# Optimization experiments

Hardware: AMD Instinct MI355X
Metric: run time of the kernel (lower is better)

Reference implementation:

```python
import jax, jax.numpy as jnp
import numpy as np

N_USER, N_PC, N_URL = 200000, 50000, 100000
E_USES, E_VISITS = 1000000, 1000000
H = 64
NUM_LAYERS = 2


def setup_inputs() -> dict:
    key = jax.random.key(0)
    ks = jax.random.split(key, 32)
    ki = iter(ks)

    def nrm(shape, scale=0.1):
        return jax.random.normal(next(ki), shape, dtype=jnp.float32) * scale

    inp = {
        "x_user": jax.random.normal(next(ki), (N_USER, 6), dtype=jnp.float32),
        "x_pc": jax.random.normal(next(ki), (N_PC, 4), dtype=jnp.float32),
        "x_url": jax.random.normal(next(ki), (N_URL, 3), dtype=jnp.float32),
        # edge_uses: row0 = user src ids, row1 = pc dst ids
        "edge_uses": jnp.stack([
            jax.random.randint(next(ki), (E_USES,), 0, N_USER),
            jax.random.randint(next(ki), (E_USES,), 0, N_PC),
        ]).astype(jnp.int32),
        # edge_visits: row0 = user src ids, row1 = url dst ids
        "edge_visits": jnp.stack([
            jax.random.randint(next(ki), (E_VISITS,), 0, N_USER),
            jax.random.randint(next(ki), (E_VISITS,), 0, N_URL),
        ]).astype(jnp.int32),
        # input projections (PyG Linear: y = x @ W + b)
        "Wu": nrm((6, H)), "bu": nrm((H,)),
        "Wp": nrm((4, H)), "bp": nrm((H,)),
        "Wl": nrm((3, H)), "bl": nrm((H,)),
        # per layer, per relation SAGEConv params; relation order:
        # 0: user-uses->pc, 1: pc-used_by->user, 2: user-visits->url, 3: url-visited_by->user
        "sage_l_W": nrm((NUM_LAYERS, 4, H, H)),
        "sage_l_b": nrm((NUM_LAYERS, 4, H)),
        "sage_r_W": nrm((NUM_LAYERS, 4, H, H)),
        # classifier (dropout is identity at eval)
        "cW1": nrm((H, H // 2)), "cb1": nrm((H // 2,)),
        "cW2": nrm((H // 2, 2)), "cb2": nrm((2,)),
    }
    return inp


def _sage(x_src, x_dst, src_idx, dst_idx, W_l, b_l, W_r, n_dst):
    # SAGEConv: lin_l(mean_{neighbors} x_src) + lin_r(x_dst)
    msg = x_src[src_idx]                                   # [E, H] gather
    s = jax.ops.segment_sum(msg, dst_idx, num_segments=n_dst)
    cnt = jax.ops.segment_sum(jnp.ones((src_idx.shape[0],), jnp.float32),
                              dst_idx, num_segments=n_dst)[:, None]
    mean = jnp.where(cnt > 0, s / jnp.maximum(cnt, 1.0), 0.0)
    return mean @ W_l + b_l + x_dst @ W_r


def reference(x_user, x_pc, x_url, edge_uses, edge_visits,
              Wu, bu, Wp, bp, Wl, bl,
              sage_l_W, sage_l_b, sage_r_W,
              cW1, cb1, cW2, cb2):
    hu = x_user @ Wu + bu
    hp = x_pc @ Wp + bp
    hl = x_url @ Wl + bl

    u2p_s, u2p_d = edge_uses[0], edge_uses[1]
    u2l_s, u2l_d = edge_visits[0], edge_visits[1]

    for layer in range(NUM_LAYERS):
        WL, BL, WR = sage_l_W[layer], sage_l_b[layer], sage_r_W[layer]
        new_pc = _sage(hu, hp, u2p_s, u2p_d, WL[0], BL[0], WR[0], N_PC)
        new_user = (_sage(hp, hu, u2p_d, u2p_s, WL[1], BL[1], WR[1], N_USER)
                    + _sage(hl, hu, u2l_d, u2l_s, WL[3], BL[3], WR[3], N_USER))
        new_url = _sage(hu, hl, u2l_s, u2l_d, WL[2], BL[2], WR[2], N_URL)
        hu, hp, hl = jax.nn.relu(new_user), jax.nn.relu(new_pc), jax.nn.relu(new_url)

    h = jax.nn.relu(hu @ cW1 + cb1)
    return h @ cW2 + cb2
```

## Files before the change

kernel.cpp:

```cpp
#include <hip/hip_runtime.h>

typedef __attribute__((ext_vector_type(8))) short bf16x8;
typedef __attribute__((ext_vector_type(4))) float f32x4;
typedef __attribute__((ext_vector_type(4))) int i32x4;
typedef unsigned short u16;

constexpr int NUSER = 200000;
constexpr int NPC   = 50000;
constexpr int NURL  = 100000;
constexpr int EUSES = 1000000;
constexpr int EVIS  = 1000000;
constexpr int HD    = 64;
constexpr int ETOT2 = 2 * (EUSES + EVIS);

constexpr int SB_P  = 0;
constexpr int SB_U1 = NPC;
constexpr int SB_L  = NPC + NUSER;
constexpr int SB_U2 = NPC + NUSER + NURL;
constexpr int NTOT  = NPC + NUSER + NURL + NUSER;

constexpr int CAP_P = 56;
constexpr int CAP_U = 28;
constexpr int CAP_L = 36;

constexpr int NBIN  = 128;
constexpr int NBINS = 512;
constexpr int NSCB  = 256;
constexpr int NSCAN = NBINS * NSCB;

__device__ __forceinline__ int binOfP(int k) { return (k * NBIN) / NPC; }
__device__ __forceinline__ int binOfU(int k) { return (k * NBIN) / NUSER; }
__device__ __forceinline__ int binOfL(int k) { return (k * NBIN) / NURL; }

__device__ __forceinline__ u16 f2bf(float f) {
    union { float f; unsigned u; } v; v.f = f;
    unsigned r = v.u + 0x7fff + ((v.u >> 16) & 1);
    return (u16)(r >> 16);
}
__device__ __forceinline__ float bf2f(u16 b) {
    union { unsigned u; float f; } v; v.u = ((unsigned)b) << 16; return v.f;
}
__device__ __forceinline__ void acc8(float* a, uint4 v) {
    unsigned w0 = v.x, w1 = v.y, w2 = v.z, w3 = v.w;
    a[0] += bf2f((u16)(w0 & 0xffff)); a[1] += bf2f((u16)(w0 >> 16));
    a[2] += bf2f((u16)(w1 & 0xffff)); a[3] += bf2f((u16)(w1 >> 16));
    a[4] += bf2f((u16)(w2 & 0xffff)); a[5] += bf2f((u16)(w2 >> 16));
    a[6] += bf2f((u16)(w3 & 0xffff)); a[7] += bf2f((u16)(w3 >> 16));
}


__global__ __launch_bounds__(256) void proj_k(
    const float* __restrict__ x, const float* __restrict__ W,
    const float* __restrict__ b, u16* __restrict__ h,
    int n, int din)
{
    int id = blockIdx.x * 256 + threadIdx.x;
    int node = id >> 6, c = id & 63;
    if (node >= n) return;
    float acc = b[c];
    for (int k = 0; k < din; ++k)
        acc += x[node * din + k] * W[k * 64 + c];
    h[id] = f2bf(acc);
}

__global__ __launch_bounds__(256) void bin_count_k(
    const int* __restrict__ eu, const int* __restrict__ ev,
    int* __restrict__ blockCnt)
{
    __shared__ int hist[NBINS];
    int tid = threadIdx.x;
    for (int i = tid; i < NBINS; i += 256) hist[i] = 0;
    __syncthreads();
    int stride = gridDim.x * 256;
    for (int e = blockIdx.x * 256 + tid; e < EUSES; e += stride) {
        int s = __builtin_nontemporal_load(eu + e);
        int d = __builtin_nontemporal_load(eu + EUSES + e);
        atomicAdd(&hist[binOfP(d)], 1);
        atomicAdd(&hist[NBIN + binOfU(s)], 1);
    }
    for (int e = blockIdx.x * 256 + tid; e < EVIS; e += stride) {
        int s = __builtin_nontemporal_load(ev + e);
        int d = __builtin_nontemporal_load(ev + EVIS + e);
        atomicAdd(&hist[2 * NBIN + binOfL(d)], 1);
        atomicAdd(&hist[3 * NBIN + binOfU(s)], 1);
    }
    __syncthreads();
    for (int i = tid; i < NBINS; i += 256)
        blockCnt[i * NSCB + blockIdx.x] = hist[i];
}

__global__ __launch_bounds__(256) void scanA_k(
    const int* __restrict__ in, int* __restrict__ out,
    int* __restrict__ bsum, int n)
{
    __shared__ int lds[256];
    int b = blockIdx.x, t = threadIdx.x;
    int base = b * 1024 + t * 4;
    int v[4]; int s = 0;
    #pragma unroll
    for (int i = 0; i < 4; ++i) { v[i] = (base + i < n) ? in[base + i] : 0; s += v[i]; }
    int x = s;
    lds[t] = x; __syncthreads();
    for (int off = 1; off < 256; off <<= 1) {
        int y = (t >= off) ? lds[t - off] : 0;
        __syncthreads();
        x += y; lds[t] = x;
        __syncthreads();
    }
    int excl = x - s;
    #pragma unroll
    for (int i = 0; i < 4; ++i) { if (base + i < n) out[base + i] = excl; excl += v[i]; }
    if (t == 255) bsum[b] = x;
}

__global__ __launch_bounds__(256) void scanB_k(int* __restrict__ bsum, int nb)
{
    __shared__ int lds[256];
    int t = threadIdx.x;
    int carry = 0;
    for (int base = 0; base < nb; base += 256) {
        int i = base + t;
        int s = (i < nb) ? bsum[i] : 0;
        int x = s;
        lds[t] = x; __syncthreads();
        for (int off = 1; off < 256; off <<= 1) {
            int y = (t >= off) ? lds[t - off] : 0;
            __syncthreads();
            x += y; lds[t] = x;
            __syncthreads();
        }
        if (i < nb) bsum[i] = carry + x - s;
        int tot = lds[255];
        __syncthreads();
        carry += tot;
    }
}

__global__ __launch_bounds__(256) void scanC_k(
    int* __restrict__ out, const int* __restrict__ bsum, int n)
{
    int i = blockIdx.x * 256 + threadIdx.x;
    if (i >= n) return;
    out[i] += bsum[i >> 10];
}

__global__ __launch_bounds__(256) void bin_scatter_k(
    const int* __restrict__ eu, const int* __restrict__ ev,
    const int* __restrict__ blockScan, int2* __restrict__ binned)
{
    __shared__ int base[NBINS];
    __shared__ int cur[NBINS];
    int tid = threadIdx.x;
    for (int i = tid; i < NBINS; i += 256) {
        base[i] = blockScan[i * NSCB + blockIdx.x];
        cur[i] = 0;
    }
    __syncthreads();
    int stride = gridDim.x * 256;
    for (int e = blockIdx.x * 256 + tid; e < EUSES; e += stride) {
        int s = __builtin_nontemporal_load(eu + e);
        int d = __builtin_nontemporal_load(eu + EUSES + e);
        int b0 = binOfP(d);
        int r0 = atomicAdd(&cur[b0], 1);
        binned[(size_t)base[b0] + r0] = make_int2(d, s);
        int b1 = NBIN + binOfU(s);
        int r1 = atomicAdd(&cur[b1], 1);
        binned[(size_t)base[b1] + r1] = make_int2(s, d);
    }
    for (int e = blockIdx.x * 256 + tid; e < EVIS; e += stride) {
        int s = __builtin_nontemporal_load(ev + e);
        int d = __builtin_nontemporal_load(ev + EVIS + e);
        int b2 = 2 * NBIN + binOfL(d);
        int r2 = atomicAdd(&cur[b2], 1);
        binned[(size_t)base[b2] + r2] = make_int2(d, s);
        int b3 = 3 * NBIN + binOfU(s);
        int r3 = atomicAdd(&cur[b3], 1);
        binned[(size_t)base[b3] + r3] = make_int2(s, d);
    }
}

__global__ __launch_bounds__(256) void bucket_build_k(
    const int2* __restrict__ binned, const int* __restrict__ blockScan,
    int* __restrict__ deg,
    int* __restrict__ colP, int* __restrict__ colU1,
    int* __restrict__ colL, int* __restrict__ colU2)
{
    __shared__ int ldsDeg[1568];
    int bin = blockIdx.x;
    int rel = bin >> 7, sub = bin & (NBIN - 1);
    int tid = threadIdx.x;
    int range, slot0, cap;
    int* col;
    if (rel == 0)      { range = NPC;   slot0 = SB_P;  col = colP;  cap = CAP_P; }
    else if (rel == 1) { range = NUSER; slot0 = SB_U1; col = colU1; cap = CAP_U; }
    else if (rel == 2) { range = NURL;  slot0 = SB_L;  col = colL;  cap = CAP_L; }
    else               { range = NUSER; slot0 = SB_U2; col = colU2; cap = CAP_U; }
    int lo = (sub * range + NBIN - 1) / NBIN;
    int hi = ((sub + 1) * range + NBIN - 1) / NBIN;
    int nk = hi - lo;
    for (int i = tid; i < nk; i += 256) ldsDeg[i] = 0;
    __syncthreads();
    int b0 = blockScan[bin * NSCB];
    int bend = (bin == NBINS - 1) ? ETOT2 : blockScan[(bin + 1) * NSCB];
    int cnt = bend - b0;
    for (int i = tid; i < cnt; i += 256) {
        int2 kp = binned[(size_t)b0 + i];
        int r = atomicAdd(&ldsDeg[kp.x - lo], 1);
        if (r < cap) col[(size_t)kp.x * cap + r] = kp.y;
    }
    __syncthreads();
    for (int i = tid; i < nk; i += 256) deg[slot0 + lo + i] = ldsDeg[i];
}

__global__ __launch_bounds__(256) void gather_all_k(
    const u16* __restrict__ hu, const u16* __restrict__ hp,
    const u16* __restrict__ hl,
    const int* __restrict__ colP, const int* __restrict__ colU1,
    const int* __restrict__ colL, const int* __restrict__ colU2,
    const int* __restrict__ deg, u16* __restrict__ meanAll)
{
    int t = blockIdx.x * 256 + threadIdx.x;
    int slot = t >> 3;
    if (slot >= NTOT) return;
    int lane8 = (t & 7) << 3;
    const u16* hsrc;
    const int* col;
    int cap;
    if (slot < SB_U1)      { hsrc = hu; col = colP  + (size_t)(slot)         * CAP_P; cap = CAP_P; }
    else if (slot < SB_L)  { hsrc = hp; col = colU1 + (size_t)(slot - SB_U1) * CAP_U; cap = CAP_U; }
    else if (slot < SB_U2) { hsrc = hu; col = colL  + (size_t)(slot - SB_L)  * CAP_L; cap = CAP_L; }
    else                   { hsrc = hl; col = colU2 + (size_t)(slot - SB_U2) * CAP_U; cap = CAP_U; }
    int dg = deg[slot];
    int m_n = dg < cap ? dg : cap;
    float a[8] = {0.f,0.f,0.f,0.f,0.f,0.f,0.f,0.f};
    const i32x4* colv = (const i32x4*)col;
    int nb = m_n >> 2, rem = m_n & 3;
    if (m_n > 0) {
        i32x4 c = __builtin_nontemporal_load(colv);
        for (int b = 0; b < nb; ++b) {
            i32x4 cn = __builtin_nontemporal_load(colv + b + 1);
            uint4 v0 = *(const uint4*)(hsrc + (size_t)c[0] * 64 + lane8);
            uint4 v1 = *(const uint4*)(hsrc + (size_t)c[1] * 64 + lane8);
            uint4 v2 = *(const uint4*)(hsrc + (size_t)c[2] * 64 + lane8);
            uint4 v3 = *(const uint4*)(hsrc + (size_t)c[3] * 64 + lane8);
            acc8(a, v0); acc8(a, v1); acc8(a, v2); acc8(a, v3);
            c = cn;
        }
        if (rem > 0) { uint4 v = *(const uint4*)(hsrc + (size_t)c[0] * 64 + lane8); acc8(a, v); }
        if (rem > 1) { uint4 v = *(const uint4*)(hsrc + (size_t)c[1] * 64 + lane8); acc8(a, v); }
        if (rem > 2) { uint4 v = *(const uint4*)(hsrc + (size_t)c[2] * 64 + lane8); acc8(a, v); }
    }
    float inv = dg > 0 ? 1.f / (float)dg : 0.f;
    uint4 m;
    m.x = (unsigned)f2bf(a[0] * inv) | ((unsigned)f2bf(a[1] * inv) << 16);
    m.y = (unsigned)f2bf(a[2] * inv) | ((unsigned)f2bf(a[3] * inv) << 16);
    m.z = (unsigned)f2bf(a[4] * inv) | ((unsigned)f2bf(a[5] * inv) << 16);
    m.w = (unsigned)f2bf(a[6] * inv) | ((unsigned)f2bf(a[7] * inv) << 16);
    *(uint4*)(meanAll + (size_t)slot * 64 + lane8) = m;
}

__global__ __launch_bounds__(256) void btprep_k(
    const float* __restrict__ lW, const float* __restrict__ lB,
    const float* __restrict__ rW,
    u16* __restrict__ bt, float* __restrict__ bias)
{
    int idx = blockIdx.x * 256 + threadIdx.x;
    if (idx < 57344) {
        int layer = idx / 28672, rem = idx % 28672;
        size_t wb = (size_t)layer * 4 * 4096;
        int n, k, K; float val; u16* out;
        if (rem < 8192) {
            K = 128; n = rem >> 7; k = rem & 127;
            val = k < 64 ? lW[wb + 0 * 4096 + k * 64 + n]
                         : rW[wb + 0 * 4096 + (k - 64) * 64 + n];
            out = bt + (size_t)layer * 28672;
        } else if (rem < 16384) {
            int e = rem - 8192; K = 128; n = e >> 7; k = e & 127;
            val = k < 64 ? lW[wb + 2 * 4096 + k * 64 + n]
                         : rW[wb + 2 * 4096 + (k - 64) * 64 + n];
            out = bt + (size_t)layer * 28672 + 8192;
        } else {
            int e = rem - 16384; K = 192; n = e / 192; k = e % 192;
            if (k < 64)       val = lW[wb + 1 * 4096 + k * 64 + n];
            else if (k < 128) val = lW[wb + 3 * 4096 + (k - 64) * 64 + n];
            else              val = rW[wb + 1 * 4096 + (k - 128) * 64 + n]
                                  + rW[wb + 3 * 4096 + (k - 128) * 64 + n];
            out = bt + (size_t)layer * 28672 + 16384;
        }
        int byte = n * (2 * K) + 2 * k;
        byte ^= ((n & 7) << 4);
        out[byte >> 1] = f2bf(val);
    } else if (idx < 57728) {
        int i2 = idx - 57344;
        int layer = i2 / 192, r = i2 % 192, which = r / 64, c = r % 64;
        size_t bb = (size_t)layer * 4 * 64;
        float v;
        if (which == 0)      v = lB[bb + 0 * 64 + c];
        else if (which == 1) v = lB[bb + 2 * 64 + c];
        else                 v = lB[bb + 1 * 64 + c] + lB[bb + 3 * 64 + c];
        bias[(layer * 3 + which) * 64 + c] = v;
    }
}

template<int STEPS>
__global__ __launch_bounds__(256) void sage_mfma_k(
    const u16* __restrict__ src0, const u16* __restrict__ src1,
    const u16* __restrict__ src2, u16* __restrict__ hout,
    const u16* __restrict__ Bt, const float* __restrict__ bias, int n)
{
    constexpr int K = STEPS * 32;
    __shared__ u16 sB[64 * K];
    int tid = threadIdx.x;
    for (int i = tid; i < 64 * K / 8; i += 256)
        ((uint4*)sB)[i] = ((const uint4*)Bt)[i];
    __syncthreads();

    int lane = tid & 63, wave = tid >> 6;
    int row0 = blockIdx.x * 64 + wave * 16;
    int arow = row0 + (lane & 15);
    int kq = (lane >> 4) * 8;
    bool rowok = arow < n;

    const u16* srcs[3] = {src0, src1, src2};
    f32x4 acc0 = {0.f,0.f,0.f,0.f}, acc1 = acc0, acc2 = acc0, acc3 = acc0;
    f32x4* acc[4] = {&acc0, &acc1, &acc2, &acc3};

    #pragma unroll
    for (int s = 0; s < STEPS; ++s) {
        const u16* sp = srcs[s >> 1];
        int klocal = (s & 1) * 32 + kq;
        bf16x8 afrag = {0,0,0,0,0,0,0,0};
        if (rowok) afrag = *(const bf16x8*)(sp + (size_t)arow * 64 + klocal);
        int kk = s * 32 + kq;
        #pragma unroll
        for (int t = 0; t < 4; ++t) {
            int colc = t * 16 + (lane & 15);
            int byte = colc * (2 * K) + kk * 2;
            byte ^= ((colc & 7) << 4);
            bf16x8 bfrag = *(const bf16x8*)((const char*)sB + byte);
            *acc[t] = __builtin_amdgcn_mfma_f32_16x16x32_bf16(afrag, bfrag, *acc[t], 0, 0, 0);
        }
    }

    #pragma unroll
    for (int t = 0; t < 4; ++t) {
        int colc = t * 16 + (lane & 15);
        float bs = bias[colc];
        #pragma unroll
        for (int r = 0; r < 4; ++r) {
            int row = row0 + (lane >> 4) * 4 + r;
            if (row < n)
                hout[(size_t)row * 64 + colc] = f2bf(fmaxf((*acc[t])[r] + bs, 0.f));
        }
    }
}

__global__ __launch_bounds__(256) void classifier_k(
    const u16* __restrict__ hu,
    const float* __restrict__ cW1, const float* __restrict__ cb1,
    const float* __restrict__ cW2, const float* __restrict__ cb2,
    float* __restrict__ out, int n)
{
    __shared__ float sW1[64 * 32];
    __shared__ float sX[32][65];
    __shared__ float sHid[32][33];
    __shared__ float sW2[64];
    __shared__ float sb1[32];
    __shared__ float sb2[2];
    int tid = threadIdx.x;
    for (int i = tid; i < 2048; i += 256) sW1[i] = cW1[i];
    if (tid < 64) sW2[tid] = cW2[tid];
    if (tid < 32) sb1[tid] = cb1[tid];
    if (tid < 2)  sb2[tid] = cb2[tid];
    int row0 = blockIdx.x * 32;
    {
        int r = tid >> 3, k8 = (tid & 7) * 8;
        int gr = row0 + r;
        if (gr < n) {
            uint4 v = *(const uint4*)(hu + (size_t)gr * 64 + k8);
            unsigned w[4] = {v.x, v.y, v.z, v.w};
            #pragma unroll
            for (int j = 0; j < 4; ++j) {
                sX[r][k8 + 2 * j]     = bf2f((u16)(w[j] & 0xffff));
                sX[r][k8 + 2 * j + 1] = bf2f((u16)(w[j] >> 16));
            }
        } else {
            #pragma unroll
            for (int j = 0; j < 8; ++j) sX[r][k8 + j] = 0.f;
        }
    }
    __syncthreads();
    int c  = tid & 31;
    int rb = tid >> 5;
    for (int r = rb; r < 32; r += 8) {
        float acc = sb1[c];
        #pragma unroll
        for (int k = 0; k < 64; ++k) acc += sX[r][k] * sW1[k * 32 + c];
        sHid[r][c] = fmaxf(acc, 0.f);
    }
    __syncthreads();
    if (tid < 64) {
        int r = tid >> 1, j = tid & 1;
        int gr = row0 + r;
        if (gr < n) {
            float acc = sb2[j];
            #pragma unroll
            for (int k = 0; k < 32; ++k) acc += sHid[r][k] * sW2[k * 2 + j];
            out[gr * 2 + j] = acc;
        }
    }
}

extern "C" void kernel_launch(void* const* d_in, const int* in_sizes, int n_in,
                              void* d_out, int out_size, void* d_ws, size_t ws_size,
                              hipStream_t stream)
{
    const float* x_user = (const float*)d_in[0];
    const float* x_pc   = (const float*)d_in[1];
    const float* x_url  = (const float*)d_in[2];
    const int*   e_uses = (const int*)d_in[3];
    const int*   e_vis  = (const int*)d_in[4];
    const float* Wu = (const float*)d_in[5];
    const float* bu = (const float*)d_in[6];
    const float* Wp = (const float*)d_in[7];
    const float* bp = (const float*)d_in[8];
    const float* Wl = (const float*)d_in[9];
    const float* bl = (const float*)d_in[10];
    const float* sage_l_W = (const float*)d_in[11];
    const float* sage_l_b = (const float*)d_in[12];
    const float* sage_r_W = (const float*)d_in[13];
    const float* cW1 = (const float*)d_in[14];
    const float* cb1 = (const float*)d_in[15];
    const float* cW2 = (const float*)d_in[16];
    const float* cb2 = (const float*)d_in[17];
    float* out = (float*)d_out;

    char* p = (char*)d_ws;
    auto alloc = [&](size_t bytes) { char* r = p; p += (bytes + 255) & ~(size_t)255; return r; };
    u16* hu      = (u16*)alloc((size_t)NUSER * HD * 2);
    u16* hp      = (u16*)alloc((size_t)NPC * HD * 2);
    u16* hl      = (u16*)alloc((size_t)NURL * HD * 2);
    u16* meanAll = (u16*)alloc((size_t)NTOT * HD * 2);
    u16* btbuf   = (u16*)alloc((size_t)2 * 28672 * 2);
    float* biasbuf = (float*)alloc((size_t)2 * 3 * 64 * 4);
    int* deg     = (int*)alloc((size_t)NTOT * 4);
    int* colP    = (int*)alloc((size_t)NPC   * CAP_P * 4 + 128);
    int* colU1   = (int*)alloc((size_t)NUSER * CAP_U * 4 + 128);
    int* colL    = (int*)alloc((size_t)NURL  * CAP_L * 4 + 128);
    int* colU2   = (int*)alloc((size_t)NUSER * CAP_U * 4 + 128);
    int* blockCnt  = (int*)alloc((size_t)NSCAN * 4);
    int* blockScan = (int*)alloc((size_t)NSCAN * 4);
    int* bsum      = (int*)alloc((size_t)256 * 4);
    int2* binned   = (int2*)alloc((size_t)ETOT2 * 8);

    u16* meanP  = meanAll + (size_t)SB_P  * HD;
    u16* meanU1 = meanAll + (size_t)SB_U1 * HD;
    u16* meanL  = meanAll + (size_t)SB_L  * HD;
    u16* meanU2 = meanAll + (size_t)SB_U2 * HD;

    bin_count_k<<<NSCB, 256, 0, stream>>>(e_uses, e_vis, blockCnt);
    scanA_k<<<NSCAN / 1024, 256, 0, stream>>>(blockCnt, blockScan, bsum, NSCAN);
    scanB_k<<<1, 256, 0, stream>>>(bsum, NSCAN / 1024);
    scanC_k<<<NSCAN / 256, 256, 0, stream>>>(blockScan, bsum, NSCAN);
    bin_scatter_k<<<NSCB, 256, 0, stream>>>(e_uses, e_vis, blockScan, binned);
    bucket_build_k<<<NBINS, 256, 0, stream>>>(
        binned, blockScan, deg, colP, colU1, colL, colU2);

    btprep_k<<<(57728 + 255) / 256, 256, 0, stream>>>(
        sage_l_W, sage_l_b, sage_r_W, btbuf, biasbuf);
    proj_k<<<(NUSER * 64 + 255) / 256, 256, 0, stream>>>(x_user, Wu, bu, hu, NUSER, 6);
    proj_k<<<(NPC   * 64 + 255) / 256, 256, 0, stream>>>(x_pc,   Wp, bp, hp, NPC,   4);
    proj_k<<<(NURL  * 64 + 255) / 256, 256, 0, stream>>>(x_url,  Wl, bl, hl, NURL,  3);

    for (int layer = 0; layer < 2; ++layer) {
        const u16* btP = btbuf + (size_t)layer * 28672;
        const u16* btL = btP + 8192;
        const u16* btU = btP + 16384;
        const float* bsP = biasbuf + (layer * 3 + 0) * 64;
        const float* bsL = biasbuf + (layer * 3 + 1) * 64;
        const float* bsU = biasbuf + (layer * 3 + 2) * 64;

        gather_all_k<<<(NTOT * 8 + 255) / 256, 256, 0, stream>>>(
            hu, hp, hl, colP, colU1, colL, colU2, deg, meanAll);

        sage_mfma_k<4><<<(NPC + 63) / 64, 256, 0, stream>>>(
            meanP, hp, hp, hp, btP, bsP, NPC);
        sage_mfma_k<4><<<(NURL + 63) / 64, 256, 0, stream>>>(
            meanL, hl, hl, hl, btL, bsL, NURL);
        sage_mfma_k<6><<<(NUSER + 63) / 64, 256, 0, stream>>>(
            meanU1, meanU2, hu, hu, btU, bsU, NUSER);
    }

    classifier_k<<<(NUSER + 31) / 32, 256, 0, stream>>>(
        hu, cW1, cb1, cW2, cb2, out, NUSER);
}
```

Baseline: 488.8 us.

## Fuse projection and per-layer SAGE launches, pack binned edges into 32 bits

The three input-projection launches become one kernel that branches per node type. The three per-layer SAGE MFMA launches become one kernel that picks the relation by block id. The binned edge buffer now stores each edge as a single 32-bit word, a bin-local key offset in the high bits and an 18-bit source id in the low bits. This halves the scatter and bucket traffic and removes launch overhead, at the cost of a shared LDS allocation sized for the largest relation, which may reduce occupancy for the smaller relations.

Result: faster. 456.2 us (-6.7%).

```diff
diff --git a/kernel.cpp b/kernel.cpp
--- a/kernel.cpp
+++ b/kernel.cpp
@@ -4,6 +4,7 @@
 typedef __attribute__((ext_vector_type(4))) float f32x4;
 typedef __attribute__((ext_vector_type(4))) int i32x4;
 typedef unsigned short u16;
+typedef unsigned int u32;
 
 constexpr int NUSER = 200000;
 constexpr int NPC   = 50000;
@@ -28,6 +29,11 @@
 constexpr int NSCB  = 256;
 constexpr int NSCAN = NBINS * NSCB;
 
+constexpr int NBLK_P = (NPC + 63) / 64;
+constexpr int NBLK_L = (NURL + 63) / 64;
+constexpr int NBLK_U = (NUSER + 63) / 64;
+constexpr int NBLK_TOT = NBLK_P + NBLK_L + NBLK_U;
+
 __device__ __forceinline__ int binOfP(int k) { return (k * NBIN) / NPC; }
 __device__ __forceinline__ int binOfU(int k) { return (k * NBIN) / NUSER; }
 __device__ __forceinline__ int binOfL(int k) { return (k * NBIN) / NURL; }
@@ -49,18 +55,26 @@
 }
 
 
-__global__ __launch_bounds__(256) void proj_k(
-    const float* __restrict__ x, const float* __restrict__ W,
-    const float* __restrict__ b, u16* __restrict__ h,
-    int n, int din)
+__global__ __launch_bounds__(256) void proj_all_k(
+    const float* __restrict__ xu, const float* __restrict__ xp,
+    const float* __restrict__ xl,
+    const float* __restrict__ Wu, const float* __restrict__ bu,
+    const float* __restrict__ Wp, const float* __restrict__ bp,
+    const float* __restrict__ Wl, const float* __restrict__ bl,
+    u16* __restrict__ hu, u16* __restrict__ hp, u16* __restrict__ hl)
 {
     int id = blockIdx.x * 256 + threadIdx.x;
     int node = id >> 6, c = id & 63;
-    if (node >= n) return;
+    const float* x; const float* W; const float* b; u16* h; int din;
+    if (node < NUSER) { x = xu + (size_t)node * 6; W = Wu; b = bu; h = hu + (size_t)node * 64; din = 6; }
+    else if (node < NUSER + NPC) {
+        int m = node - NUSER; x = xp + (size_t)m * 4; W = Wp; b = bp; h = hp + (size_t)m * 64; din = 4;
+    } else if (node < NUSER + NPC + NURL) {
+        int m = node - NUSER - NPC; x = xl + (size_t)m * 3; W = Wl; b = bl; h = hl + (size_t)m * 64; din = 3;
+    } else return;
     float acc = b[c];
-    for (int k = 0; k < din; ++k)
-        acc += x[node * din + k] * W[k * 64 + c];
-    h[id] = f2bf(acc);
+    for (int k = 0; k < din; ++k) acc += x[k] * W[k * 64 + c];
+    h[c] = f2bf(acc);
 }
 
 __global__ __launch_bounds__(256) void bin_count_k(
@@ -146,14 +160,18 @@
 
 __global__ __launch_bounds__(256) void bin_scatter_k(
     const int* __restrict__ eu, const int* __restrict__ ev,
-    const int* __restrict__ blockScan, int2* __restrict__ binned)
+    const int* __restrict__ blockScan, u32* __restrict__ binned)
 {
     __shared__ int base[NBINS];
     __shared__ int cur[NBINS];
+    __shared__ int lo[NBINS];
     int tid = threadIdx.x;
     for (int i = tid; i < NBINS; i += 256) {
         base[i] = blockScan[i * NSCB + blockIdx.x];
         cur[i] = 0;
+        int rel = i >> 7, sub = i & (NBIN - 1);
+        int range = (rel == 0) ? NPC : (rel == 2) ? NURL : NUSER;
+        lo[i] = (sub * range + NBIN - 1) / NBIN;
     }
     __syncthreads();
     int stride = gridDim.x * 256;
@@ -162,25 +180,25 @@
         int d = __builtin_nontemporal_load(eu + EUSES + e);
         int b0 = binOfP(d);
         int r0 = atomicAdd(&cur[b0], 1);
-        binned[(size_t)base[b0] + r0] = make_int2(d, s);
+        binned[(size_t)base[b0] + r0] = ((u32)(d - lo[b0]) << 18) | (u32)s;
         int b1 = NBIN + binOfU(s);
         int r1 = atomicAdd(&cur[b1], 1);
-        binned[(size_t)base[b1] + r1] = make_int2(s, d);
+        binned[(size_t)base[b1] + r1] = ((u32)(s - lo[b1]) << 18) | (u32)d;
     }
     for (int e = blockIdx.x * 256 + tid; e < EVIS; e += stride) {
         int s = __builtin_nontemporal_load(ev + e);
         int d = __builtin_nontemporal_load(ev + EVIS + e);
         int b2 = 2 * NBIN + binOfL(d);
         int r2 = atomicAdd(&cur[b2], 1);
-        binned[(size_t)base[b2] + r2] = make_int2(d, s);
+        binned[(size_t)base[b2] + r2] = ((u32)(d - lo[b2]) << 18) | (u32)s;
         int b3 = 3 * NBIN + binOfU(s);
         int r3 = atomicAdd(&cur[b3], 1);
-        binned[(size_t)base[b3] + r3] = make_int2(s, d);
+        binned[(size_t)base[b3] + r3] = ((u32)(s - lo[b3]) << 18) | (u32)d;
     }
 }
 
 __global__ __launch_bounds__(256) void bucket_build_k(
-    const int2* __restrict__ binned, const int* __restrict__ blockScan,
+    const u32* __restrict__ binned, const int* __restrict__ blockScan,
     int* __restrict__ deg,
     int* __restrict__ colP, int* __restrict__ colU1,
     int* __restrict__ colL, int* __restrict__ colU2)
@@ -204,9 +222,11 @@
     int bend = (bin == NBINS - 1) ? ETOT2 : blockScan[(bin + 1) * NSCB];
     int cnt = bend - b0;
     for (int i = tid; i < cnt; i += 256) {
-        int2 kp = binned[(size_t)b0 + i];
-        int r = atomicAdd(&ldsDeg[kp.x - lo], 1);
-        if (r < cap) col[(size_t)kp.x * cap + r] = kp.y;
+        u32 w = binned[(size_t)b0 + i];
+        int local = (int)(w >> 18);
+        int payload = (int)(w & 0x3FFFFu);
+        int r = atomicAdd(&ldsDeg[local], 1);
+        if (r < cap) col[(size_t)(lo + local) * cap + r] = payload;
     }
     __syncthreads();
     for (int i = tid; i < nk; i += 256) deg[slot0 + lo + i] = ldsDeg[i];
@@ -303,21 +323,20 @@
 }
 
 template<int STEPS>
-__global__ __launch_bounds__(256) void sage_mfma_k(
+__device__ __forceinline__ void sage_body(
     const u16* __restrict__ src0, const u16* __restrict__ src1,
     const u16* __restrict__ src2, u16* __restrict__ hout,
-    const u16* __restrict__ Bt, const float* __restrict__ bias, int n)
+    const u16* __restrict__ Bt, const float* __restrict__ bias,
+    int n, int row0, u16* sB, int tid)
 {
     constexpr int K = STEPS * 32;
-    __shared__ u16 sB[64 * K];
-    int tid = threadIdx.x;
     for (int i = tid; i < 64 * K / 8; i += 256)
         ((uint4*)sB)[i] = ((const uint4*)Bt)[i];
     __syncthreads();
 
     int lane = tid & 63, wave = tid >> 6;
-    int row0 = blockIdx.x * 64 + wave * 16;
-    int arow = row0 + (lane & 15);
+    int wrow0 = row0 + wave * 16;
+    int arow = wrow0 + (lane & 15);
     int kq = (lane >> 4) * 8;
     bool rowok = arow < n;
 
@@ -348,10 +367,32 @@
         float bs = bias[colc];
         #pragma unroll
         for (int r = 0; r < 4; ++r) {
-            int row = row0 + (lane >> 4) * 4 + r;
+            int row = wrow0 + (lane >> 4) * 4 + r;
             if (row < n)
                 hout[(size_t)row * 64 + colc] = f2bf(fmaxf((*acc[t])[r] + bs, 0.f));
         }
+    }
+}
+
+__global__ __launch_bounds__(256) void sage_layer_k(
+    const u16* __restrict__ meanAll,
+    u16* __restrict__ hu, u16* __restrict__ hp, u16* __restrict__ hl,
+    const u16* __restrict__ btL0, const float* __restrict__ biasL0)
+{
+    __shared__ u16 sB[64 * 192];
+    int bid = blockIdx.x, tid = threadIdx.x;
+    const u16* meanP  = meanAll + (size_t)SB_P  * HD;
+    const u16* meanU1 = meanAll + (size_t)SB_U1 * HD;
+    const u16* meanL  = meanAll + (size_t)SB_L  * HD;
+    const u16* meanU2 = meanAll + (size_t)SB_U2 * HD;
+    if (bid < NBLK_P) {
+        sage_body<4>(meanP, hp, hp, hp, btL0, biasL0, NPC, bid * 64, sB, tid);
+    } else if (bid < NBLK_P + NBLK_L) {
+        sage_body<4>(meanL, hl, hl, hl, btL0 + 8192, biasL0 + 64,
+                     NURL, (bid - NBLK_P) * 64, sB, tid);
+    } else {
+        sage_body<6>(meanU1, meanU2, hu, hu, btL0 + 16384, biasL0 + 128,
+                     NUSER, (bid - NBLK_P - NBLK_L) * 64, sB, tid);
     }
 }
 
@@ -451,12 +492,7 @@
     int* blockCnt  = (int*)alloc((size_t)NSCAN * 4);
     int* blockScan = (int*)alloc((size_t)NSCAN * 4);
     int* bsum      = (int*)alloc((size_t)256 * 4);
-    int2* binned   = (int2*)alloc((size_t)ETOT2 * 8);
-
-    u16* meanP  = meanAll + (size_t)SB_P  * HD;
-    u16* meanU1 = meanAll + (size_t)SB_U1 * HD;
-    u16* meanL  = meanAll + (size_t)SB_L  * HD;
-    u16* meanU2 = meanAll + (size_t)SB_U2 * HD;
+    u32* binned    = (u32*)alloc((size_t)ETOT2 * 4);
 
     bin_count_k<<<NSCB, 256, 0, stream>>>(e_uses, e_vis, blockCnt);
     scanA_k<<<NSCAN / 1024, 256, 0, stream>>>(blockCnt, blockScan, bsum, NSCAN);
@@ -468,27 +504,15 @@
 
     btprep_k<<<(57728 + 255) / 256, 256, 0, stream>>>(
         sage_l_W, sage_l_b, sage_r_W, btbuf, biasbuf);
-    proj_k<<<(NUSER * 64 + 255) / 256, 256, 0, stream>>>(x_user, Wu, bu, hu, NUSER, 6);
-    proj_k<<<(NPC   * 64 + 255) / 256, 256, 0, stream>>>(x_pc,   Wp, bp, hp, NPC,   4);
-    proj_k<<<(NURL  * 64 + 255) / 256, 256, 0, stream>>>(x_url,  Wl, bl, hl, NURL,  3);
+    proj_all_k<<<((NUSER + NPC + NURL) * 64 + 255) / 256, 256, 0, stream>>>(
+        x_user, x_pc, x_url, Wu, bu, Wp, bp, Wl, bl, hu, hp, hl);
 
     for (int layer = 0; layer < 2; ++layer) {
-        const u16* btP = btbuf + (size_t)layer * 28672;
-        const u16* btL = btP + 8192;
-        const u16* btU = btP + 16384;
-        const float* bsP = biasbuf + (layer * 3 + 0) * 64;
-        const float* bsL = biasbuf + (layer * 3 + 1) * 64;
-        const float* bsU = biasbuf + (layer * 3 + 2) * 64;
-
         gather_all_k<<<(NTOT * 8 + 255) / 256, 256, 0, stream>>>(
             hu, hp, hl, colP, colU1, colL, colU2, deg, meanAll);
-
-        sage_mfma_k<4><<<(NPC + 63) / 64, 256, 0, stream>>>(
-            meanP, hp, hp, hp, btP, bsP, NPC);
-        sage_mfma_k<4><<<(NURL + 63) / 64, 256, 0, stream>>>(
-            meanL, hl, hl, hl, btL, bsL, NURL);
-        sage_mfma_k<6><<<(NUSER + 63) / 64, 256, 0, stream>>>(
-            meanU1, meanU2, hu, hu, btU, bsU, NUSER);
+        sage_layer_k<<<NBLK_TOT, 256, 0, stream>>>(
+            meanAll, hu, hp, hl,
+            btbuf + (size_t)layer * 28672, biasbuf + (size_t)layer * 3 * 64);
     }
 
     classifier_k<<<(NUSER + 31) / 32, 256, 0, stream>>>(
```
